# Kernel optimization log

Hardware: AMD Instinct MI355X
Metric: run time of the kernel (lower is better)

The kernel has to match this reference:

```python
import jax, jax.numpy as jnp
import numpy as np

B, S, D, H = 2, 2048, 1024, 16
DH = D // H


def setup_inputs() -> dict:
    key = jax.random.key(0)
    ks = jax.random.split(key, 13)
    s = 1.0 / np.sqrt(D)
    inp = {
        "q": jax.random.normal(ks[0], (B, S, D), jnp.float32),
        "k": jax.random.normal(ks[1], (B, S, D), jnp.float32),
        "v": jax.random.normal(ks[2], (B, S, D), jnp.float32),
        # causal mask [B,1,Q,K]: True = attend
        "attn_mask": jnp.broadcast_to(jnp.tril(jnp.ones((S, S), bool))[None, None], (B, 1, S, S)),
        "rel_bias": 0.1 * jax.random.normal(ks[3], (H, S, S), jnp.float32),
        "Wq": s * jax.random.normal(ks[4], (D, D), jnp.float32),
        "bq": jnp.zeros((D,), jnp.float32),
        "Wk": s * jax.random.normal(ks[5], (D, D), jnp.float32),
        "bk": jnp.zeros((D,), jnp.float32),
        "Wv": s * jax.random.normal(ks[6], (D, D), jnp.float32),
        "bv": jnp.zeros((D,), jnp.float32),
        "Wo": s * jax.random.normal(ks[7], (D, D), jnp.float32),
        "bo": jnp.zeros((D,), jnp.float32),
    }
    return inp


def reference(q, k, v, attn_mask, rel_bias, Wq, bq, Wk, bk, Wv, bv, Wo, bo):
    Bq, Q, Dm = q.shape
    K = k.shape[1]
    # projections -> [B, H, S, DH]
    qh = (q @ Wq + bq).reshape(Bq, Q, H, DH).transpose(0, 2, 1, 3)
    kh = (k @ Wk + bk).reshape(Bq, K, H, DH).transpose(0, 2, 1, 3)
    vh = (v @ Wv + bv).reshape(Bq, K, H, DH).transpose(0, 2, 1, 3)
    scores = jnp.einsum("bhqd,bhkd->bhqk", qh, kh) / np.sqrt(DH).astype(np.float32)
    scores = scores + rel_bias  # [H,Q,K] broadcasts over batch
    scores = jnp.where(attn_mask, scores, -jnp.inf)
    attn = jax.nn.softmax(scores, axis=-1)
    out = jnp.einsum("bhqk,bhkd->bhqd", attn, vh)
    out = out.transpose(0, 2, 1, 3).reshape(Bq, Q, Dm)
    return out @ Wo + bo
```

## Files before the change

kernel.cpp:

```cpp
#include <hip/hip_runtime.h>

typedef unsigned short u16;
typedef __attribute__((ext_vector_type(8))) short bf16x8;
typedef __attribute__((ext_vector_type(4))) float f32x4;
typedef __attribute__((ext_vector_type(4))) unsigned short us4;

#define B_ 2
#define S_ 2048
#define D_ 1024
#define H_ 16
#define DH_ 64
#define M_ 4096

__device__ __forceinline__ u16 f2bf(float f) {
  unsigned int u = __builtin_bit_cast(unsigned int, f);
  u += 0x7FFFu + ((u >> 16) & 1u);
  return (u16)(u >> 16);
}

__device__ __forceinline__ void gload_lds16(const void* g, void* l) {
  __builtin_amdgcn_global_load_lds(
      (__attribute__((address_space(1))) void*)(g),
      (__attribute__((address_space(3))) void*)(l),
      16, 0, 0);
}

__global__ __launch_bounds__(256) void wprep_kernel(const float* __restrict__ W0,
                                                    const float* __restrict__ W1,
                                                    const float* __restrict__ W2,
                                                    const float* __restrict__ W3,
                                                    u16* __restrict__ Wt,
                                                    const float* __restrict__ qin,
                                                    const float* __restrict__ kin,
                                                    const float* __restrict__ vin,
                                                    u16* __restrict__ Xq,
                                                    u16* __restrict__ Xk,
                                                    u16* __restrict__ Xv) {
  int z = blockIdx.z;
  if (z < 4) {
    __shared__ float tile[32][33];
    const float* W = (z == 0) ? W0 : (z == 1) ? W1 : (z == 2) ? W2 : W3;
    u16* out = Wt + (size_t)z * D_ * D_;
    int tx = threadIdx.x, ty = threadIdx.y;
    int x = blockIdx.x * 32 + tx;
    for (int j = 0; j < 32; j += 8)
      tile[ty + j][tx] = W[(size_t)(blockIdx.y * 32 + ty + j) * D_ + x];
    __syncthreads();
    int x2 = blockIdx.y * 32 + tx;
    for (int j = 0; j < 32; j += 8)
      out[(size_t)(blockIdx.x * 32 + ty + j) * D_ + x2] = f2bf(tile[tx][ty + j]);
  } else {
    int zz = z - 4;
    const float* src = (zz == 0) ? qin : (zz == 1) ? kin : vin;
    u16* dst = (zz == 0) ? Xq : (zz == 1) ? Xk : Xv;
    int bid = blockIdx.y * 32 + blockIdx.x;
    int t = threadIdx.y * 32 + threadIdx.x;
    const float4* s4 = (const float4*)src;
    for (int i = 0; i < 4; ++i) {
      int idx = bid * 1024 + i * 256 + t;
      float4 v4 = s4[idx];
      us4 o;
      o[0] = f2bf(v4.x); o[1] = f2bf(v4.y); o[2] = f2bf(v4.z); o[3] = f2bf(v4.w);
      ((us4*)dst)[idx] = o;
    }
  }
}

__global__ __launch_bounds__(256) void gemm_qkv(const u16* __restrict__ Xq,
                                                const u16* __restrict__ Xk,
                                                const u16* __restrict__ Xv,
                                                const u16* __restrict__ Wt,
                                                const float* __restrict__ bq,
                                                const float* __restrict__ bk,
                                                const float* __restrict__ bv,
                                                u16* __restrict__ Qh,
                                                u16* __restrict__ Kh,
                                                u16* __restrict__ Vt) {
  __shared__ u16 As[128 * 32];
  __shared__ u16 Bs[128 * 32];
  int fid = blockIdx.x;
  int xcd = fid & 7, ii = fid >> 3;
  int grp = ii >> 3, yy = ii & 7;
  int gg = xcd * 12 + grp;
  int z = gg >> 5;
  int xx = gg & 31;
  const u16* A = (z == 0) ? Xq : (z == 1) ? Xk : Xv;
  const u16* Bt = Wt + (size_t)z * D_ * D_;
  const float* bias = (z == 0) ? bq : (z == 1) ? bk : bv;
  u16* O = (z == 0) ? Qh : (z == 1) ? Kh : Vt;

  int tid = threadIdx.x;
  int lane = tid & 63, wave = tid >> 6;
  int m0 = xx * 128, n0 = yy * 128;
  int wr = wave >> 1, wc = wave & 1;
  int fr = lane & 15, fk = (lane >> 4) * 8;

  f32x4 acc[4][4];
  const f32x4 vzero = {0.f, 0.f, 0.f, 0.f};
  for (int i = 0; i < 4; ++i)
    for (int j = 0; j < 4; ++j) acc[i][j] = vzero;

  for (int k0 = 0; k0 < D_; k0 += 32) {
    if (k0) __syncthreads();
    for (int i = 0; i < 2; ++i) {
      int wofs = ((i * 4 + wave) << 10);
      int ofs = wofs + lane * 16;
      int row = ofs >> 6;
      int cole = (ofs & 63) >> 1;
      gload_lds16(A + (size_t)(m0 + row) * D_ + k0 + cole, (char*)As + wofs);
      gload_lds16(Bt + (size_t)(n0 + row) * D_ + k0 + cole, (char*)Bs + wofs);
    }
    __syncthreads();
    bf16x8 af[4], bfr[4];
    for (int mi = 0; mi < 4; ++mi)
      af[mi] = *(const bf16x8*)(As + (wr * 64 + mi * 16 + fr) * 32 + fk);
    for (int ni = 0; ni < 4; ++ni)
      bfr[ni] = *(const bf16x8*)(Bs + (wc * 64 + ni * 16 + fr) * 32 + fk);
    for (int mi = 0; mi < 4; ++mi)
      for (int ni = 0; ni < 4; ++ni)
        acc[mi][ni] =
            __builtin_amdgcn_mfma_f32_16x16x32_bf16(af[mi], bfr[ni], acc[mi][ni], 0, 0, 0);
  }

  if (z == 2) {
    for (int mi = 0; mi < 4; ++mi) {
      int rowb = m0 + wr * 64 + mi * 16 + (lane >> 4) * 4;
      int bb2 = rowb >> 11, s0 = rowb & (S_ - 1);
      for (int ni = 0; ni < 4; ++ni) {
        int col = n0 + wc * 64 + ni * 16 + fr;
        int hh = col >> 6, dh = col & 63;
        float bv = bias[col];
        us4 pk;
        for (int r = 0; r < 4; ++r) pk[r] = f2bf(acc[mi][ni][r] + bv);
        *(us4*)(O + ((size_t)(bb2 * H_ + hh) * DH_ + dh) * S_ + s0) = pk;
      }
    }
  } else {
    float scale = (z == 0) ? 0.125f : 1.0f;
    for (int mi = 0; mi < 4; ++mi) {
      int rowb = m0 + wr * 64 + mi * 16 + (lane >> 4) * 4;
      for (int ni = 0; ni < 4; ++ni) {
        int col = n0 + wc * 64 + ni * 16 + fr;
        int hh = col >> 6, dh = col & 63;
        float bv = bias[col];
        for (int r = 0; r < 4; ++r) {
          int row = rowb + r;
          int bb2 = row >> 11, s = row & (S_ - 1);
          O[((size_t)(bb2 * H_ + hh) * S_ + s) * DH_ + dh] =
              f2bf((acc[mi][ni][r] + bv) * scale);
        }
      }
    }
  }
}

__global__ __launch_bounds__(256) void gemm_out(const u16* __restrict__ A,
                                                const u16* __restrict__ Bt,
                                                const float* __restrict__ bias,
                                                float* __restrict__ O) {
  __shared__ u16 As[64 * 32];
  __shared__ u16 Bs[128 * 32];
  int fid = blockIdx.x;
  int xcd = fid & 7, ii = fid >> 3;
  int grp = ii >> 3, yy = ii & 7;
  int gg = xcd * 8 + grp;
  int tid = threadIdx.x;
  int lane = tid & 63, wave = tid >> 6;
  int m0 = gg * 64, n0 = yy * 128;
  int fr = lane & 15, fk = (lane >> 4) * 8;

  f32x4 acc[4][2];
  const f32x4 vzero = {0.f, 0.f, 0.f, 0.f};
  for (int i = 0; i < 4; ++i)
    for (int j = 0; j < 2; ++j) acc[i][j] = vzero;

  for (int k0 = 0; k0 < D_; k0 += 32) {
    if (k0) __syncthreads();
    {
      int wofs = wave << 10;
      int ofs = wofs + lane * 16;
      int row = ofs >> 6;
      int cole = (ofs & 63) >> 1;
      gload_lds16(A + (size_t)(m0 + row) * D_ + k0 + cole, (char*)As + wofs);
    }
    for (int i = 0; i < 2; ++i) {
      int wofs = ((i * 4 + wave) << 10);
      int ofs = wofs + lane * 16;
      int row = ofs >> 6;
      int cole = (ofs & 63) >> 1;
      gload_lds16(Bt + (size_t)(n0 + row) * D_ + k0 + cole, (char*)Bs + wofs);
    }
    __syncthreads();
    bf16x8 af[4], bfr[2];
    for (int mi = 0; mi < 4; ++mi)
      af[mi] = *(const bf16x8*)(As + (mi * 16 + fr) * 32 + fk);
    for (int ni = 0; ni < 2; ++ni)
      bfr[ni] = *(const bf16x8*)(Bs + (wave * 32 + ni * 16 + fr) * 32 + fk);
    for (int mi = 0; mi < 4; ++mi)
      for (int ni = 0; ni < 2; ++ni)
        acc[mi][ni] =
            __builtin_amdgcn_mfma_f32_16x16x32_bf16(af[mi], bfr[ni], acc[mi][ni], 0, 0, 0);
  }

  for (int mi = 0; mi < 4; ++mi) {
    int rowb = m0 + mi * 16 + (lane >> 4) * 4;
    for (int ni = 0; ni < 2; ++ni) {
      int col = n0 + wave * 32 + ni * 16 + fr;
      float bv = bias[col];
      for (int r = 0; r < 4; ++r)
        O[(size_t)(rowb + r) * D_ + col] = acc[mi][ni][r] + bv;
    }
  }
}

__global__ __launch_bounds__(256, 4) void attn_kernel(const u16* __restrict__ Qh,
                                                      const u16* __restrict__ Kh,
                                                      const u16* __restrict__ Vt,
                                                      const float* __restrict__ relb,
                                                      u16* __restrict__ attnout) {
  __shared__ u16 KVs[2][2][4096];

  int fid = blockIdx.x;
  int b = (fid >> 3) & 1;
  int rest = (fid >> 4) * 8 + (fid & 7);
  int h = rest & 15;
  int s = 31 - (rest >> 4);

  int w = threadIdx.x >> 6, lane = threadIdx.x & 63;
  int fr = lane & 15, g = lane >> 4;
  int q0w = s * 64 + w * 16;
  int qme = q0w + fr;
  int bh = b * H_ + h;
  int sx = (fr & 7) << 4;

  int kind = w >> 1;
  int i0 = (w & 1) * 4;
  int srow_lo = lane >> 3;
  int scb = (lane & 7) * 16;

  const u16* Qb = Qh + ((size_t)bh * S_ + q0w) * DH_;
  bf16x8 qf0 = *(const bf16x8*)(Qb + fr * DH_ + 8 * g);
  bf16x8 qf1 = *(const bf16x8*)(Qb + fr * DH_ + 32 + 8 * g);

  const float* Bq = relb + (size_t)h * S_ * S_ + (size_t)qme * S_ + 4 * g;
  const f32x4 vzero = {0.f, 0.f, 0.f, 0.f};

  int T = s + 1;

  auto STAGE = [&](int buf, int kb) {
    for (int i = 0; i < 4; ++i) {
      int ii = i0 + i;
      int row = ii * 8 + srow_lo;
      int cbs = scb ^ ((row & 7) << 4);
      const u16* src;
      if (kind == 0)
        src = Kh + ((size_t)bh * S_ + kb + row) * DH_ + (cbs >> 1);
      else
        src = Vt + ((size_t)bh * DH_ + row) * S_ + kb + (cbs >> 1);
      gload_lds16(src, &KVs[kind][buf][ii * 512]);
    }
  };

  f32x4 acc[4];
  for (int f4 = 0; f4 < 4; ++f4) acc[f4] = vzero;
  float m = -1.0e4f, l = 0.f;

  STAGE(0, 0);
  f32x4 bi[4], bn[4];
  for (int c = 0; c < 4; ++c) bi[c] = *(const f32x4*)(Bq + 16 * c);
  __syncthreads();

  for (int t = 0; t < T; ++t) {
    int kb = t * 64;
    int buf = t & 1;
    if (t + 1 < T) {
      STAGE(buf ^ 1, kb + 64);
      for (int c = 0; c < 4; ++c) bn[c] = *(const f32x4*)(Bq + kb + 64 + 16 * c);
    }

    const u16* Kt = &KVs[0][buf][0];
    const u16* Vl = &KVs[1][buf][0];

    f32x4 sc[4];
    __builtin_amdgcn_s_setprio(1);
    for (int c = 0; c < 4; ++c) {
      bf16x8 k0 = *(const bf16x8*)(Kt + (16 * c + fr) * 64 + (((16 * g) ^ sx) >> 1));
      bf16x8 k1 = *(const bf16x8*)(Kt + (16 * c + fr) * 64 + (((64 + 16 * g) ^ sx) >> 1));
      f32x4 z = vzero;
      z = __builtin_amdgcn_mfma_f32_16x16x32_bf16(k0, qf0, z, 0, 0, 0);
      z = __builtin_amdgcn_mfma_f32_16x16x32_bf16(k1, qf1, z, 0, 0, 0);
      sc[c] = z;
    }
    __builtin_amdgcn_s_setprio(0);
    for (int c = 0; c < 4; ++c)
      for (int r = 0; r < 4; ++r) {
        int key = kb + 16 * c + 4 * g + r;
        sc[c][r] = (key <= qme) ? sc[c][r] + bi[c][r] : -1e30f;
      }
    float pm = sc[0][0];
    for (int c = 0; c < 4; ++c)
      for (int r = 0; r < 4; ++r) pm = fmaxf(pm, sc[c][r]);
    pm = fmaxf(pm, __shfl_xor(pm, 16));
    pm = fmaxf(pm, __shfl_xor(pm, 32));
    if (!__all(pm - m <= 8.0f)) {
      float mn = fmaxf(m, pm);
      float corr = __expf(m - mn);
      m = mn;
      l *= corr;
      float c0 = __shfl(corr, 4 * g + 0);
      float c1 = __shfl(corr, 4 * g + 1);
      float c2 = __shfl(corr, 4 * g + 2);
      float c3 = __shfl(corr, 4 * g + 3);
      for (int f4 = 0; f4 < 4; ++f4) {
        acc[f4][0] *= c0; acc[f4][1] *= c1; acc[f4][2] *= c2; acc[f4][3] *= c3;
      }
    }
    float rs = 0.f;
    for (int c = 0; c < 4; ++c)
      for (int r = 0; r < 4; ++r) {
        sc[c][r] = __expf(sc[c][r] - m);
        rs += sc[c][r];
      }
    rs += __shfl_xor(rs, 16);
    rs += __shfl_xor(rs, 32);
    l += rs;
    union { u16 u[8]; bf16x8 v; } pp[2];
    for (int j = 0; j < 2; ++j)
      for (int r = 0; r < 4; ++r) {
        pp[j].u[r] = f2bf(sc[2 * j][r]);
        pp[j].u[4 + r] = f2bf(sc[2 * j + 1][r]);
      }
    __builtin_amdgcn_s_setprio(1);
    for (int f4 = 0; f4 < 4; ++f4) {
      for (int j = 0; j < 2; ++j) {
        union { us4 hh[2]; bf16x8 v; } vf;
        vf.hh[0] = *(const us4*)(Vl + (f4 * 16 + fr) * 64 + (((j * 64 + 8 * g) ^ sx) >> 1));
        vf.hh[1] = *(const us4*)(Vl + (f4 * 16 + fr) * 64 + (((j * 64 + 32 + 8 * g) ^ sx) >> 1));
        acc[f4] = __builtin_amdgcn_mfma_f32_16x16x32_bf16(pp[j].v, vf.v, acc[f4], 0, 0, 0);
      }
    }
    __builtin_amdgcn_s_setprio(0);
    for (int c = 0; c < 4; ++c) bi[c] = bn[c];
    __syncthreads();
  }

  float il = 1.f / l;
  for (int r = 0; r < 4; ++r) {
    float ilr = __shfl(il, 4 * g + r);
    int qq = q0w + 4 * g + r;
    u16* ob = attnout + ((size_t)b * S_ + qq) * D_ + h * 64;
    for (int f4 = 0; f4 < 4; ++f4) ob[f4 * 16 + fr] = f2bf(acc[f4][r] * ilr);
  }
}

extern "C" void kernel_launch(void* const* d_in, const int* in_sizes, int n_in,
                              void* d_out, int out_size, void* d_ws, size_t ws_size,
                              hipStream_t stream) {
  const float* q = (const float*)d_in[0];
  const float* k = (const float*)d_in[1];
  const float* v = (const float*)d_in[2];
  const float* rb = (const float*)d_in[4];
  const float* Wq = (const float*)d_in[5];
  const float* bq = (const float*)d_in[6];
  const float* Wk = (const float*)d_in[7];
  const float* bk = (const float*)d_in[8];
  const float* Wv = (const float*)d_in[9];
  const float* bv = (const float*)d_in[10];
  const float* Wo = (const float*)d_in[11];
  const float* bo = (const float*)d_in[12];
  float* out = (float*)d_out;

  char* ws = (char*)d_ws;
  const size_t SZ = (size_t)M_ * D_ * 2;
  u16* Xq = (u16*)(ws);
  u16* Xk = (u16*)(ws + SZ);
  u16* Xv = (u16*)(ws + 2 * SZ);
  u16* Qh = (u16*)(ws + 3 * SZ);
  u16* Kh = (u16*)(ws + 4 * SZ);
  u16* Vt = (u16*)(ws + 5 * SZ);
  u16* Wt = (u16*)(ws + 6 * SZ);
  u16* Xb = Xq;

  wprep_kernel<<<dim3(32, 32, 7), dim3(32, 8), 0, stream>>>(Wq, Wk, Wv, Wo, Wt,
                                                            q, k, v, Xq, Xk, Xv);

  gemm_qkv<<<dim3(768), 256, 0, stream>>>(Xq, Xk, Xv, Wt, bq, bk, bv, Qh, Kh, Vt);

  attn_kernel<<<dim3(1024), 256, 0, stream>>>(Qh, Kh, Vt, rb, Xb);

  gemm_out<<<dim3(512), 256, 0, stream>>>(Xb, Wt + 3 * (size_t)D_ * D_, bo, out);
}
```

Measured before the change: 160.9 us.

## Skip causal masking off-diagonal, defer row-sum reduction, pack bf16 conversion, remap blocks

The attention kernel now applies the causal mask only on the final diagonal key tile and simply adds the bias on all other tiles. It moves the cross-lane row-sum shuffles out of the loop to a single reduction at the end, which is valid because the rescale factor is uniform across the reduced lanes. It also converts probabilities to bf16 with the packed v_cvt_pk_bf16_f32 instruction and changes the block-to-(b,h,s) mapping to pair heavy and light causal query tiles. Together these cut per-tile VALU work and rebalance load across workgroups. The new mapping changes scheduling order and may affect cache locality for the relative-bias reads.

```diff
diff --git a/kernel.cpp b/kernel.cpp
--- a/kernel.cpp
+++ b/kernel.cpp
@@ -16,6 +16,12 @@
   unsigned int u = __builtin_bit_cast(unsigned int, f);
   u += 0x7FFFu + ((u >> 16) & 1u);
   return (u16)(u >> 16);
+}
+
+__device__ __forceinline__ unsigned int cvtpk(float lo, float hi) {
+  unsigned int r;
+  asm("v_cvt_pk_bf16_f32 %0, %1, %2" : "=v"(r) : "v"(lo), "v"(hi));
+  return r;
 }
 
 __device__ __forceinline__ void gload_lds16(const void* g, void* l) {
@@ -221,10 +227,11 @@
   __shared__ u16 KVs[2][2][4096];
 
   int fid = blockIdx.x;
-  int b = (fid >> 3) & 1;
-  int rest = (fid >> 4) * 8 + (fid & 7);
-  int h = rest & 15;
-  int s = 31 - (rest >> 4);
+  int rr = fid >> 8, c = fid & 255;
+  int j = c >> 3, e = c & 7;
+  int s = (rr & 1) ? j : 31 - j;
+  int h = (rr & 1) ? e + 8 : e;
+  int b = rr >> 1;
 
   int w = threadIdx.x >> 6, lane = threadIdx.x & 63;
   int fr = lane & 15, g = lane >> 4;
@@ -267,15 +274,16 @@
 
   STAGE(0, 0);
   f32x4 bi[4], bn[4];
-  for (int c = 0; c < 4; ++c) bi[c] = *(const f32x4*)(Bq + 16 * c);
+  for (int cc = 0; cc < 4; ++cc) bi[cc] = *(const f32x4*)(Bq + 16 * cc);
   __syncthreads();
 
   for (int t = 0; t < T; ++t) {
     int kb = t * 64;
     int buf = t & 1;
-    if (t + 1 < T) {
+    bool diag = (t == T - 1);
+    if (!diag) {
       STAGE(buf ^ 1, kb + 64);
-      for (int c = 0; c < 4; ++c) bn[c] = *(const f32x4*)(Bq + kb + 64 + 16 * c);
+      for (int cc = 0; cc < 4; ++cc) bn[cc] = *(const f32x4*)(Bq + kb + 64 + 16 * cc);
     }
 
     const u16* Kt = &KVs[0][buf][0];
@@ -283,23 +291,28 @@
 
     f32x4 sc[4];
     __builtin_amdgcn_s_setprio(1);
-    for (int c = 0; c < 4; ++c) {
-      bf16x8 k0 = *(const bf16x8*)(Kt + (16 * c + fr) * 64 + (((16 * g) ^ sx) >> 1));
-      bf16x8 k1 = *(const bf16x8*)(Kt + (16 * c + fr) * 64 + (((64 + 16 * g) ^ sx) >> 1));
+    for (int cc = 0; cc < 4; ++cc) {
+      bf16x8 k0 = *(const bf16x8*)(Kt + (16 * cc + fr) * 64 + (((16 * g) ^ sx) >> 1));
+      bf16x8 k1 = *(const bf16x8*)(Kt + (16 * cc + fr) * 64 + (((64 + 16 * g) ^ sx) >> 1));
       f32x4 z = vzero;
       z = __builtin_amdgcn_mfma_f32_16x16x32_bf16(k0, qf0, z, 0, 0, 0);
       z = __builtin_amdgcn_mfma_f32_16x16x32_bf16(k1, qf1, z, 0, 0, 0);
-      sc[c] = z;
+      sc[cc] = z;
     }
     __builtin_amdgcn_s_setprio(0);
-    for (int c = 0; c < 4; ++c)
-      for (int r = 0; r < 4; ++r) {
-        int key = kb + 16 * c + 4 * g + r;
-        sc[c][r] = (key <= qme) ? sc[c][r] + bi[c][r] : -1e30f;
-      }
+    if (diag) {
+      for (int cc = 0; cc < 4; ++cc)
+        for (int r = 0; r < 4; ++r) {
+          int key = kb + 16 * cc + 4 * g + r;
+          sc[cc][r] = (key <= qme) ? sc[cc][r] + bi[cc][r] : -1e30f;
+        }
+    } else {
+      for (int cc = 0; cc < 4; ++cc)
+        for (int r = 0; r < 4; ++r) sc[cc][r] += bi[cc][r];
+    }
     float pm = sc[0][0];
-    for (int c = 0; c < 4; ++c)
-      for (int r = 0; r < 4; ++r) pm = fmaxf(pm, sc[c][r]);
+    for (int cc = 0; cc < 4; ++cc)
+      for (int r = 0; r < 4; ++r) pm = fmaxf(pm, sc[cc][r]);
     pm = fmaxf(pm, __shfl_xor(pm, 16));
     pm = fmaxf(pm, __shfl_xor(pm, 32));
     if (!__all(pm - m <= 8.0f)) {
@@ -316,34 +329,35 @@
       }
     }
     float rs = 0.f;
-    for (int c = 0; c < 4; ++c)
+    for (int cc = 0; cc < 4; ++cc)
       for (int r = 0; r < 4; ++r) {
-        sc[c][r] = __expf(sc[c][r] - m);
-        rs += sc[c][r];
+        sc[cc][r] = __expf(sc[cc][r] - m);
+        rs += sc[cc][r];
       }
-    rs += __shfl_xor(rs, 16);
-    rs += __shfl_xor(rs, 32);
     l += rs;
-    union { u16 u[8]; bf16x8 v; } pp[2];
-    for (int j = 0; j < 2; ++j)
-      for (int r = 0; r < 4; ++r) {
-        pp[j].u[r] = f2bf(sc[2 * j][r]);
-        pp[j].u[4 + r] = f2bf(sc[2 * j + 1][r]);
-      }
+    union { unsigned int w4[4]; bf16x8 v; } pp[2];
+    for (int jj = 0; jj < 2; ++jj) {
+      pp[jj].w4[0] = cvtpk(sc[2 * jj][0], sc[2 * jj][1]);
+      pp[jj].w4[1] = cvtpk(sc[2 * jj][2], sc[2 * jj][3]);
+      pp[jj].w4[2] = cvtpk(sc[2 * jj + 1][0], sc[2 * jj + 1][1]);
+      pp[jj].w4[3] = cvtpk(sc[2 * jj + 1][2], sc[2 * jj + 1][3]);
+    }
     __builtin_amdgcn_s_setprio(1);
     for (int f4 = 0; f4 < 4; ++f4) {
-      for (int j = 0; j < 2; ++j) {
+      for (int jj = 0; jj < 2; ++jj) {
         union { us4 hh[2]; bf16x8 v; } vf;
-        vf.hh[0] = *(const us4*)(Vl + (f4 * 16 + fr) * 64 + (((j * 64 + 8 * g) ^ sx) >> 1));
-        vf.hh[1] = *(const us4*)(Vl + (f4 * 16 + fr) * 64 + (((j * 64 + 32 + 8 * g) ^ sx) >> 1));
-        acc[f4] = __builtin_amdgcn_mfma_f32_16x16x32_bf16(pp[j].v, vf.v, acc[f4], 0, 0, 0);
+        vf.hh[0] = *(const us4*)(Vl + (f4 * 16 + fr) * 64 + (((jj * 64 + 8 * g) ^ sx) >> 1));
+        vf.hh[1] = *(const us4*)(Vl + (f4 * 16 + fr) * 64 + (((jj * 64 + 32 + 8 * g) ^ sx) >> 1));
+        acc[f4] = __builtin_amdgcn_mfma_f32_16x16x32_bf16(pp[jj].v, vf.v, acc[f4], 0, 0, 0);
       }
     }
     __builtin_amdgcn_s_setprio(0);
-    for (int c = 0; c < 4; ++c) bi[c] = bn[c];
+    for (int cc = 0; cc < 4; ++cc) bi[cc] = bn[cc];
     __syncthreads();
   }
 
+  l += __shfl_xor(l, 16);
+  l += __shfl_xor(l, 32);
   float il = 1.f / l;
   for (int r = 0; r < 4; ++r) {
     float ilr = __shfl(il, 4 * g + r);
```

Measured after the change: 142.1 us. 11.7% less time.
